# Kernel optimization log

Hardware: AMD Instinct MI355X
Metric: run time of the kernel (lower is better)

## Reference

```python
import jax, jax.numpy as jnp
import numpy as np

SIGMA = 10.0
# 24 neighbor offsets: all (dh, dw) in [-2,2]^2 except (0,0)
OFFSETS = [(dh, dw) for dh in range(-2, 3) for dw in range(-2, 3) if not (dh == 0 and dw == 0)]


def rgb2ycbcr(x):
    # x: [B,3,H,W]; flat @ mat + bias, exactly as the torch module (mat as written)
    mat = jnp.array([[0.257, -0.148, 0.439],
                     [0.564, -0.291, -0.368],
                     [0.098, 0.439, -0.071]], dtype=x.dtype)
    bias = jnp.array([16 / 255.0, 128 / 255.0, 128 / 255.0], dtype=x.dtype)
    # bchw -> bhwc contraction with mat, then back to bchw
    return jnp.einsum('bchw,ck->bkhw', x, mat) + bias[None, :, None, None]


def shifted_diff(a, dh, dw):
    # a[..., shifted slice] - a[..., opposite slice]; matches torch slicing exactly
    H, W = a.shape[-2], a.shape[-1]
    h1s, h1e = max(dh, 0), H + min(dh, 0)
    w1s, w1e = max(dw, 0), W + min(dw, 0)
    h2s, h2e = max(-dh, 0), H + min(-dh, 0)
    w2s, w2e = max(-dw, 0), W + min(-dw, 0)
    return a[..., h1s:h1e, w1s:w1e] - a[..., h2s:h2e, w2s:w2e]


def setup_inputs() -> dict:
    key = jax.random.key(0)
    k1, k2 = jax.random.split(key)
    B, C, H, W = 16, 3, 512, 512
    inp = jax.random.uniform(k1, (B, C, H, W), dtype=jnp.float32)
    out = jax.random.uniform(k2, (B, C, H, W), dtype=jnp.float32)
    return {"input": inp, "output": out}


def reference(input, output):
    x = rgb2ycbcr(input)
    y = output
    s = -1.0 / (2.0 * SIGMA * SIGMA)
    total = jnp.zeros((), dtype=x.dtype)
    for dh, dw in OFFSETS:
        dx = shifted_diff(x, dh, dw)
        dy = shifted_diff(y, dh, dw)
        w = jnp.exp(jnp.sum(dx * dx, axis=1, keepdims=True) * s)  # [B,1,h,w]
        l1 = jnp.sum(jnp.abs(dy), axis=1, keepdims=True)          # [B,1,h,w]
        total = total + jnp.mean(w * l1)
    return total / len(OFFSETS)
```

## Files before the change

kernel.cpp:

```cpp
#include <hip/hip_runtime.h>
#include <hip/hip_bf16.h>
#include <stdint.h>


#define B_ 16
#define H_ 512
#define W_ 512
#define HW_ (H_ * W_)
#define CHW_ (3 * HW_)

#define TH 8
#define ROWS 10
#define COLS 520
#define NTHREADS 512
#define POISON 1e19f

__global__ void zero_out_kernel(float* p) { p[0] = 0.0f; }

__device__ __forceinline__ void gload16(const float* gsrc, float* ldst) {
  __builtin_amdgcn_global_load_lds(
      (const __attribute__((address_space(1))) void*)gsrc,
      (__attribute__((address_space(3))) void*)ldst, 16, 0, 0);
}

template <int DH, int DW>
__device__ __forceinline__ float contrib(const float (&O)[6][8], const float (&N)[6][8]) {
  constexpr int AW = DW < 0 ? -DW : DW;
  const float scale =
      2.0f / (24.0f * (float)B_ * (float)(H_ - DH) * (float)(W_ - AW));
  float s = 0.0f;
#pragma unroll
  for (int p = 0; p < 4; ++p) {
    const int ci = p + 2;
    const int ni = p + 2 + DW;
    float d0 = O[0][ci] - N[0][ni];
    float d1 = O[1][ci] - N[1][ni];
    float d2 = O[2][ci] - N[2][ni];
    float q = d0 * d0 + d1 * d1 + d2 * d2;
    float wgt = __expf(-q);
    float l1 = fabsf(O[3][ci] - N[3][ni]) + fabsf(O[4][ci] - N[4][ni]) +
               fabsf(O[5][ci] - N[5][ni]);
    s += wgt * l1;
  }
  return scale * s;
}

__global__ __launch_bounds__(NTHREADS) void smooth_loss_kernel(
    const float* __restrict__ in, const float* __restrict__ outp,
    float* __restrict__ result) {
  __shared__ float lds[6][ROWS][COLS];
  __shared__ float wsum[NTHREADS / 64];

  const int tid = threadIdx.x;
  const int wv = tid >> 6;
  const int lane = tid & 63;
  const int by = blockIdx.x;
  const int b = blockIdx.y;
  const int ibase = by * TH;

  const float* inb = in + (size_t)b * CHW_;
  const float* outb = outp + (size_t)b * CHW_;

#pragma unroll
  for (int k = 0; k < 15; ++k) {
    int c = wv + 8 * k;
    int r = c / 12;
    int rem = c - r * 12;
    int p = rem >> 1;
    int h = rem & 1;
    if (ibase + r < H_) {
      const float* src =
          (p < 3 ? inb + (size_t)p * HW_ : outb + (size_t)(p - 3) * HW_) +
          (size_t)(ibase + r) * W_ + 256 * h + 4 * lane;
      gload16(src, &lds[p][r][4 + 256 * h]);
    }
  }

  if (tid < 480) {
    int p = tid / 80;
    int rr = (tid % 80) / 8;
    int ci = tid % 8;
    int col = ci < 4 ? ci : 512 + ci;
    lds[p][rr][col] = (p == 0) ? POISON : 0.0f;
  }
  if (ibase + TH >= H_) {
    for (int c = tid; c < 6 * 2 * 130; c += NTHREADS) {
      int p = c / 260;
      int rem = c - p * 260;
      int r = 8 + rem / 130;
      int q4 = rem % 130;
      float v = (p == 0) ? POISON : 0.0f;
      *(float4*)&lds[p][r][4 * q4] = make_float4(v, v, v, v);
    }
  }

  __syncthreads();

  {
    const float K = 0.07071067811865475f;
#pragma unroll
    for (int k = 0; k < 5; ++k) {
      int c = tid + NTHREADS * k;
      int r = c >> 8;
      int c2 = c & 255;
      if (ibase + r < H_) {
        int col = 4 + 2 * c2;
        float2 rr = *(const float2*)&lds[0][r][col];
        float2 gg = *(const float2*)&lds[1][r][col];
        float2 bb = *(const float2*)&lds[2][r][col];
        float2 x0, x1, x2;
        x0.x = (0.257f * K) * rr.x + (0.564f * K) * gg.x + (0.098f * K) * bb.x;
        x0.y = (0.257f * K) * rr.y + (0.564f * K) * gg.y + (0.098f * K) * bb.y;
        x1.x = (-0.148f * K) * rr.x + (-0.291f * K) * gg.x + (0.439f * K) * bb.x;
        x1.y = (-0.148f * K) * rr.y + (-0.291f * K) * gg.y + (0.439f * K) * bb.y;
        x2.x = (0.439f * K) * rr.x + (-0.368f * K) * gg.x + (-0.071f * K) * bb.x;
        x2.y = (0.439f * K) * rr.y + (-0.368f * K) * gg.y + (-0.071f * K) * bb.y;
        *(float2*)&lds[0][r][col] = x0;
        *(float2*)&lds[1][r][col] = x1;
        *(float2*)&lds[2][r][col] = x2;
      }
    }
  }

  __syncthreads();

  float acc = 0.0f;
#pragma unroll
  for (int g = 0; g < 2; ++g) {
    const int fc = 4 * lane + 256 * g + 2;

    float O[6][8], N1[6][8], N2[6][8];
#pragma unroll
    for (int p = 0; p < 6; ++p) {
#pragma unroll
      for (int m = 0; m < 4; ++m)
        *(float2*)&O[p][2 * m] = *(const float2*)&lds[p][wv][fc + 2 * m];
    }
#pragma unroll
    for (int p = 0; p < 6; ++p) {
#pragma unroll
      for (int m = 0; m < 4; ++m)
        *(float2*)&N1[p][2 * m] = *(const float2*)&lds[p][wv + 1][fc + 2 * m];
    }
#pragma unroll
    for (int p = 0; p < 6; ++p) {
#pragma unroll
      for (int m = 0; m < 4; ++m)
        *(float2*)&N2[p][2 * m] = *(const float2*)&lds[p][wv + 2][fc + 2 * m];
    }

    acc += contrib<0, 1>(O, O);
    acc += contrib<0, 2>(O, O);
    acc += contrib<1, -2>(O, N1);
    acc += contrib<1, -1>(O, N1);
    acc += contrib<1, 0>(O, N1);
    acc += contrib<1, 1>(O, N1);
    acc += contrib<1, 2>(O, N1);
    acc += contrib<2, -2>(O, N2);
    acc += contrib<2, -1>(O, N2);
    acc += contrib<2, 0>(O, N2);
    acc += contrib<2, 1>(O, N2);
    acc += contrib<2, 2>(O, N2);
  }

#pragma unroll
  for (int o = 32; o > 0; o >>= 1) acc += __shfl_down(acc, o, 64);
  if (lane == 0) wsum[wv] = acc;
  __syncthreads();
  if (tid == 0) {
    float s = 0.0f;
#pragma unroll
    for (int wq = 0; wq < NTHREADS / 64; ++wq) s += wsum[wq];
    atomicAdd(result, s);
  }
}

extern "C" void kernel_launch(void* const* d_in, const int* in_sizes, int n_in,
                              void* d_out, int out_size, void* d_ws, size_t ws_size,
                              hipStream_t stream) {
  const float* in = (const float*)d_in[0];
  const float* outp = (const float*)d_in[1];
  float* res = (float*)d_out;

  zero_out_kernel<<<1, 1, 0, stream>>>(res);

  dim3 grid(H_ / TH, B_, 1);
  smooth_loss_kernel<<<grid, NTHREADS, 0, stream>>>(in, outp, res);
}
```

Measured before the change: 58.14 us.

## Shrink row tile to 4, widen per-thread columns to 8 with float4 LDS reads

Each block now covers 4 output rows with 256 threads instead of 8 rows with 512, and each lane handles 8 contiguous columns in a single pass rather than two passes of 4. Neighbor rows are loaded as float4 from LDS and the color-conversion pass is vectorized to float4. Launch bounds request 2 blocks per CU. This cuts LDS traffic per output and raises occupancy, at the cost of a larger halo-to-interior ratio (6 rows loaded per 4 computed) and higher register pressure.

```diff
diff --git a/kernel.cpp b/kernel.cpp
--- a/kernel.cpp
+++ b/kernel.cpp
@@ -9,10 +9,10 @@
 #define HW_ (H_ * W_)
 #define CHW_ (3 * HW_)
 
-#define TH 8
-#define ROWS 10
+#define TH 4
+#define ROWS 6
 #define COLS 520
-#define NTHREADS 512
+#define NTHREADS 256
 #define POISON 1e19f
 
 __global__ void zero_out_kernel(float* p) { p[0] = 0.0f; }
@@ -23,33 +23,52 @@
       (__attribute__((address_space(3))) void*)ldst, 16, 0, 0);
 }
 
+template <int DW>
+__device__ __forceinline__ float contrib0(const float (&O)[6][12]) {
+  const float scale =
+      2.0f / (24.0f * (float)B_ * (float)H_ * (float)(W_ - DW));
+  float s = 0.0f;
+#pragma unroll
+  for (int p = 0; p < 8; ++p) {
+    float d0 = O[0][p] - O[0][p + DW];
+    float d1 = O[1][p] - O[1][p + DW];
+    float d2 = O[2][p] - O[2][p + DW];
+    float q = d0 * d0 + d1 * d1 + d2 * d2;
+    float wgt = __expf(-q);
+    float l1 = fabsf(O[3][p] - O[3][p + DW]) + fabsf(O[4][p] - O[4][p + DW]) +
+               fabsf(O[5][p] - O[5][p + DW]);
+    s += wgt * l1;
+  }
+  return scale * s;
+}
+
 template <int DH, int DW>
-__device__ __forceinline__ float contrib(const float (&O)[6][8], const float (&N)[6][8]) {
+__device__ __forceinline__ float contribN(const float (&O)[6][12],
+                                          const float (&N)[6][16]) {
   constexpr int AW = DW < 0 ? -DW : DW;
   const float scale =
       2.0f / (24.0f * (float)B_ * (float)(H_ - DH) * (float)(W_ - AW));
   float s = 0.0f;
 #pragma unroll
-  for (int p = 0; p < 4; ++p) {
-    const int ci = p + 2;
-    const int ni = p + 2 + DW;
-    float d0 = O[0][ci] - N[0][ni];
-    float d1 = O[1][ci] - N[1][ni];
-    float d2 = O[2][ci] - N[2][ni];
+  for (int p = 0; p < 8; ++p) {
+    const int ni = p + DW + 4;
+    float d0 = O[0][p] - N[0][ni];
+    float d1 = O[1][p] - N[1][ni];
+    float d2 = O[2][p] - N[2][ni];
     float q = d0 * d0 + d1 * d1 + d2 * d2;
     float wgt = __expf(-q);
-    float l1 = fabsf(O[3][ci] - N[3][ni]) + fabsf(O[4][ci] - N[4][ni]) +
-               fabsf(O[5][ci] - N[5][ni]);
+    float l1 = fabsf(O[3][p] - N[3][ni]) + fabsf(O[4][p] - N[4][ni]) +
+               fabsf(O[5][p] - N[5][ni]);
     s += wgt * l1;
   }
   return scale * s;
 }
 
-__global__ __launch_bounds__(NTHREADS) void smooth_loss_kernel(
+__global__ __launch_bounds__(NTHREADS, 2) void smooth_loss_kernel(
     const float* __restrict__ in, const float* __restrict__ outp,
     float* __restrict__ result) {
-  __shared__ float lds[6][ROWS][COLS];
-  __shared__ float wsum[NTHREADS / 64];
+  __shared__ alignas(16) float lds[6][ROWS][COLS];
+  __shared__ float wsum[4];
 
   const int tid = threadIdx.x;
   const int wv = tid >> 6;
@@ -62,10 +81,10 @@
   const float* outb = outp + (size_t)b * CHW_;
 
 #pragma unroll
-  for (int k = 0; k < 15; ++k) {
-    int c = wv + 8 * k;
-    int r = c / 12;
-    int rem = c - r * 12;
+  for (int k = 0; k < 18; ++k) {
+    int wc = wv + 4 * k;
+    int r = wc / 12;
+    int rem = wc - 12 * r;
     int p = rem >> 1;
     int h = rem & 1;
     if (ibase + r < H_) {
@@ -76,21 +95,21 @@
     }
   }
 
-  if (tid < 480) {
-    int p = tid / 80;
-    int rr = (tid % 80) / 8;
-    int ci = tid % 8;
+  for (int it = tid; it < 288; it += NTHREADS) {
+    int p = it / 48;
+    int rem = it - 48 * p;
+    int r = rem >> 3;
+    int ci = rem & 7;
     int col = ci < 4 ? ci : 512 + ci;
-    lds[p][rr][col] = (p == 0) ? POISON : 0.0f;
+    lds[p][r][col] = (p == 0) ? POISON : 0.0f;
   }
   if (ibase + TH >= H_) {
-    for (int c = tid; c < 6 * 2 * 130; c += NTHREADS) {
-      int p = c / 260;
-      int rem = c - p * 260;
-      int r = 8 + rem / 130;
-      int q4 = rem % 130;
-      float v = (p == 0) ? POISON : 0.0f;
-      *(float4*)&lds[p][r][4 * q4] = make_float4(v, v, v, v);
+    for (int c = tid; c < 6 * 2 * COLS; c += NTHREADS) {
+      int p = c / (2 * COLS);
+      int rem = c - p * (2 * COLS);
+      int r = 4 + rem / COLS;
+      int col = rem % COLS;
+      lds[p][r][col] = (p == 0) ? POISON : 0.0f;
     }
   }
 
@@ -98,69 +117,74 @@
 
   {
     const float K = 0.07071067811865475f;
-#pragma unroll
-    for (int k = 0; k < 5; ++k) {
-      int c = tid + NTHREADS * k;
-      int r = c >> 8;
-      int c2 = c & 255;
-      if (ibase + r < H_) {
-        int col = 4 + 2 * c2;
-        float2 rr = *(const float2*)&lds[0][r][col];
-        float2 gg = *(const float2*)&lds[1][r][col];
-        float2 bb = *(const float2*)&lds[2][r][col];
-        float2 x0, x1, x2;
-        x0.x = (0.257f * K) * rr.x + (0.564f * K) * gg.x + (0.098f * K) * bb.x;
-        x0.y = (0.257f * K) * rr.y + (0.564f * K) * gg.y + (0.098f * K) * bb.y;
-        x1.x = (-0.148f * K) * rr.x + (-0.291f * K) * gg.x + (0.439f * K) * bb.x;
-        x1.y = (-0.148f * K) * rr.y + (-0.291f * K) * gg.y + (0.439f * K) * bb.y;
-        x2.x = (0.439f * K) * rr.x + (-0.368f * K) * gg.x + (-0.071f * K) * bb.x;
-        x2.y = (0.439f * K) * rr.y + (-0.368f * K) * gg.y + (-0.071f * K) * bb.y;
-        *(float2*)&lds[0][r][col] = x0;
-        *(float2*)&lds[1][r][col] = x1;
-        *(float2*)&lds[2][r][col] = x2;
+    for (int c = tid; c < ROWS * 130; c += NTHREADS) {
+      int r = c / 130;
+      int q4 = c - 130 * r;
+      int col = 4 * q4;
+      float4 rr = *(const float4*)&lds[0][r][col];
+      float4 gg = *(const float4*)&lds[1][r][col];
+      float4 bb = *(const float4*)&lds[2][r][col];
+      float rv[4] = {rr.x, rr.y, rr.z, rr.w};
+      float gv[4] = {gg.x, gg.y, gg.z, gg.w};
+      float bv[4] = {bb.x, bb.y, bb.z, bb.w};
+      float x0[4], x1[4], x2[4];
+#pragma unroll
+      for (int m = 0; m < 4; ++m) {
+        x0[m] = (0.257f * K) * rv[m] + (0.564f * K) * gv[m] + (0.098f * K) * bv[m];
+        x1[m] = (-0.148f * K) * rv[m] + (-0.291f * K) * gv[m] + (0.439f * K) * bv[m];
+        x2[m] = (0.439f * K) * rv[m] + (-0.368f * K) * gv[m] + (-0.071f * K) * bv[m];
       }
+      *(float4*)&lds[0][r][col] = make_float4(x0[0], x0[1], x0[2], x0[3]);
+      *(float4*)&lds[1][r][col] = make_float4(x1[0], x1[1], x1[2], x1[3]);
+      *(float4*)&lds[2][r][col] = make_float4(x2[0], x2[1], x2[2], x2[3]);
     }
   }
 
   __syncthreads();
 
+  const int c0 = 8 * lane;
+
   float acc = 0.0f;
-#pragma unroll
-  for (int g = 0; g < 2; ++g) {
-    const int fc = 4 * lane + 256 * g + 2;
-
-    float O[6][8], N1[6][8], N2[6][8];
-#pragma unroll
-    for (int p = 0; p < 6; ++p) {
-#pragma unroll
-      for (int m = 0; m < 4; ++m)
-        *(float2*)&O[p][2 * m] = *(const float2*)&lds[p][wv][fc + 2 * m];
-    }
-#pragma unroll
-    for (int p = 0; p < 6; ++p) {
-#pragma unroll
-      for (int m = 0; m < 4; ++m)
-        *(float2*)&N1[p][2 * m] = *(const float2*)&lds[p][wv + 1][fc + 2 * m];
-    }
-#pragma unroll
-    for (int p = 0; p < 6; ++p) {
-#pragma unroll
-      for (int m = 0; m < 4; ++m)
-        *(float2*)&N2[p][2 * m] = *(const float2*)&lds[p][wv + 2][fc + 2 * m];
-    }
-
-    acc += contrib<0, 1>(O, O);
-    acc += contrib<0, 2>(O, O);
-    acc += contrib<1, -2>(O, N1);
-    acc += contrib<1, -1>(O, N1);
-    acc += contrib<1, 0>(O, N1);
-    acc += contrib<1, 1>(O, N1);
-    acc += contrib<1, 2>(O, N1);
-    acc += contrib<2, -2>(O, N2);
-    acc += contrib<2, -1>(O, N2);
-    acc += contrib<2, 0>(O, N2);
-    acc += contrib<2, 1>(O, N2);
-    acc += contrib<2, 2>(O, N2);
+  float O[6][12];
+#pragma unroll
+  for (int p6 = 0; p6 < 6; ++p6) {
+    *(float4*)&O[p6][0] = *(const float4*)&lds[p6][wv][c0 + 4];
+    *(float4*)&O[p6][4] = *(const float4*)&lds[p6][wv][c0 + 8];
+    *(float4*)&O[p6][8] = *(const float4*)&lds[p6][wv][c0 + 12];
+  }
+
+  acc += contrib0<1>(O);
+  acc += contrib0<2>(O);
+
+  {
+    float N[6][16];
+#pragma unroll
+    for (int p6 = 0; p6 < 6; ++p6) {
+      *(float4*)&N[p6][0] = *(const float4*)&lds[p6][wv + 1][c0];
+      *(float4*)&N[p6][4] = *(const float4*)&lds[p6][wv + 1][c0 + 4];
+      *(float4*)&N[p6][8] = *(const float4*)&lds[p6][wv + 1][c0 + 8];
+      *(float4*)&N[p6][12] = *(const float4*)&lds[p6][wv + 1][c0 + 12];
+    }
+    acc += contribN<1, -2>(O, N);
+    acc += contribN<1, -1>(O, N);
+    acc += contribN<1, 0>(O, N);
+    acc += contribN<1, 1>(O, N);
+    acc += contribN<1, 2>(O, N);
+  }
+  {
+    float N[6][16];
+#pragma unroll
+    for (int p6 = 0; p6 < 6; ++p6) {
+      *(float4*)&N[p6][0] = *(const float4*)&lds[p6][wv + 2][c0];
+      *(float4*)&N[p6][4] = *(const float4*)&lds[p6][wv + 2][c0 + 4];
+      *(float4*)&N[p6][8] = *(const float4*)&lds[p6][wv + 2][c0 + 8];
+      *(float4*)&N[p6][12] = *(const float4*)&lds[p6][wv + 2][c0 + 12];
+    }
+    acc += contribN<2, -2>(O, N);
+    acc += contribN<2, -1>(O, N);
+    acc += contribN<2, 0>(O, N);
+    acc += contribN<2, 1>(O, N);
+    acc += contribN<2, 2>(O, N);
   }
 
 #pragma unroll
@@ -168,10 +192,7 @@
   if (lane == 0) wsum[wv] = acc;
   __syncthreads();
   if (tid == 0) {
-    float s = 0.0f;
-#pragma unroll
-    for (int wq = 0; wq < NTHREADS / 64; ++wq) s += wsum[wq];
-    atomicAdd(result, s);
+    atomicAdd(result, wsum[0] + wsum[1] + wsum[2] + wsum[3]);
   }
 }
 
```

After: 62.68 us. 7.8% more time.
